# Optimization experiments

Measured on AMD Instinct MI355X. Metric: run time of the kernel, lower is better.

Reference implementation:

```python
import jax, jax.numpy as jnp
import numpy as np
import math
from jax import lax

DIM = 96
D_MODEL = 2 * DIM            # SS2D d_model
D_INNER = 2 * D_MODEL        # expand = 2
D_STATE = 16
DT_RANK = math.ceil(D_MODEL / 16)
K = 4
B_, H_, W_ = 2, 48, 48


def setup_inputs() -> dict:
    key = jax.random.key(0)
    ks = jax.random.split(key, 12)
    r = lambda k, s, sc=0.02: jax.random.normal(k, s, jnp.float32) * sc
    A = np.tile(np.arange(1, D_STATE + 1, dtype=np.float32)[None, :], (K * D_INNER, 1))
    return dict(
        x=jax.random.normal(ks[0], (B_, DIM, H_, W_), jnp.float32),
        w_init=r(ks[1], (D_MODEL, DIM)),
        b_init=r(ks[2], (D_MODEL,)),
        w_fina=r(ks[3], (DIM, D_MODEL)),
        b_fina=r(ks[4], (DIM,)),
        in_proj_w=r(ks[5], (2 * D_INNER, D_MODEL)),
        conv_w=r(ks[6], (D_INNER, 1, 3, 3), 0.1),
        conv_b=r(ks[7], (D_INNER,)),
        x_proj_w=r(ks[8], (K, DT_RANK + 2 * D_STATE, D_INNER)),
        dt_w=r(ks[9], (K, D_INNER, DT_RANK), 0.1),
        dt_b=r(ks[10], (K, D_INNER), 0.1),
        A_logs=jnp.asarray(np.log(A)),
        Ds=jnp.ones((K * D_INNER,), jnp.float32),
        ln_g=jnp.ones((D_INNER,), jnp.float32),
        ln_b=jnp.zeros((D_INNER,), jnp.float32),
        out_proj_w=r(ks[11], (D_MODEL, D_INNER)),
    )


def _gelu(x):
    return jax.nn.gelu(x, approximate=False)


def _conv1x1(x, w, b):
    # x: (b,c,h,w), w: (o,c)
    return jnp.einsum('oc,bchw->bohw', w, x) + b[None, :, None, None]


def _ss2d(x, in_proj_w, conv_w, conv_b, x_proj_w, dt_w, dt_b, A_logs, Ds, ln_g, ln_b, out_proj_w):
    # x: (b, h, w, d_model)
    b, h, w, _ = x.shape
    L = h * w
    xz = jnp.einsum('bhwc,oc->bhwo', x, in_proj_w)          # (b,h,w,2*d_inner)
    xx, z = jnp.split(xz, 2, axis=-1)
    xc = xx.transpose(0, 3, 1, 2)                            # (b, d_inner, h, w)
    xc = lax.conv_general_dilated(xc, conv_w, (1, 1), 'SAME',
                                  feature_group_count=D_INNER,
                                  dimension_numbers=('NCHW', 'OIHW', 'NCHW'))
    xc = jax.nn.silu(xc + conv_b[None, :, None, None])
    # 4 scan directions: hw, wh, reversed hw, reversed wh
    x_hw = xc.reshape(b, D_INNER, L)
    x_wh = xc.transpose(0, 1, 3, 2).reshape(b, D_INNER, L)
    xs = jnp.stack([x_hw, x_wh, x_hw[..., ::-1], x_wh[..., ::-1]], axis=1)   # (b,K,d,L)
    x_dbl = jnp.einsum('bkdl,kcd->bkcl', xs, x_proj_w)
    dts = x_dbl[:, :, :DT_RANK]                               # (b,K,r,L)
    Bs = x_dbl[:, :, DT_RANK:DT_RANK + D_STATE]               # (b,K,n,L)
    Cs = x_dbl[:, :, DT_RANK + D_STATE:]                      # (b,K,n,L)
    dts = jnp.einsum('bkrl,kdr->bkdl', dts, dt_w)
    delta = jax.nn.softplus(dts + dt_b[None, :, :, None])     # (b,K,d,L)
    A = -jnp.exp(A_logs).reshape(K, D_INNER, D_STATE)         # (K,d,n)
    Dm = Ds.reshape(K, D_INNER)
    # selective scan over L (time-major stacked inputs)
    u_t = xs.transpose(3, 0, 1, 2)      # (L,b,K,d)
    dt_t = delta.transpose(3, 0, 1, 2)  # (L,b,K,d)
    B_t = Bs.transpose(3, 0, 1, 2)      # (L,b,K,n)
    C_t = Cs.transpose(3, 0, 1, 2)      # (L,b,K,n)
    h0 = jnp.zeros((b, K, D_INNER, D_STATE), xs.dtype)

    def step(hst, inp):
        u, dt, Bv, Cv = inp
        dA = jnp.exp(dt[..., None] * A)                       # (b,K,d,n)
        hst = dA * hst + (dt * u)[..., None] * Bv[:, :, None, :]
        y = jnp.einsum('bkdn,bkn->bkd', hst, Cv)
        return hst, y

    _, ys = lax.scan(step, h0, (u_t, dt_t, B_t, C_t))         # (L,b,K,d)
    ys = ys.transpose(1, 2, 3, 0) + Dm[None, :, :, None] * xs  # (b,K,d,L)
    y1 = ys[:, 0]
    y3 = ys[:, 2][..., ::-1]
    y2 = ys[:, 1].reshape(b, D_INNER, w, h).transpose(0, 1, 3, 2).reshape(b, D_INNER, L)
    y4 = ys[:, 3][..., ::-1].reshape(b, D_INNER, w, h).transpose(0, 1, 3, 2).reshape(b, D_INNER, L)
    y = (y1 + y2 + y3 + y4).transpose(0, 2, 1).reshape(b, h, w, D_INNER)
    mu = y.mean(-1, keepdims=True)
    var = y.var(-1, keepdims=True)
    y = (y - mu) / jnp.sqrt(var + 1e-5) * ln_g + ln_b
    y = y * jax.nn.silu(z)
    return jnp.einsum('bhwd,od->bhwo', y, out_proj_w)         # (b,h,w,d_model)


def _forward(x, w_init, b_init, w_fina, b_fina, in_proj_w, conv_w, conv_b,
             x_proj_w, dt_w, dt_b, A_logs, Ds, ln_g, ln_b, out_proj_w):
    x1 = _gelu(_conv1x1(x, w_init, b_init))                   # (b,2*dim,h,w)
    x0 = x1
    xt = x1.transpose(0, 2, 3, 1)                             # b h w c
    y = _ss2d(xt, in_proj_w, conv_w, conv_b, x_proj_w, dt_w, dt_b,
              A_logs, Ds, ln_g, ln_b, out_proj_w)
    y = y.transpose(0, 3, 1, 2)
    return _gelu(_conv1x1(y + x0, w_fina, b_fina))            # (b,dim,h,w)


def reference(x, w_init, b_init, w_fina, b_fina, in_proj_w, conv_w, conv_b,
              x_proj_w, dt_w, dt_b, A_logs, Ds, ln_g, ln_b, out_proj_w):
    return _forward(x, w_init, b_init, w_fina, b_fina, in_proj_w, conv_w, conv_b,
                    x_proj_w, dt_w, dt_b, A_logs, Ds, ln_g, ln_b, out_proj_w)
```

## Files before the change

kernel.cpp:

```cpp
#include <hip/hip_runtime.h>
#include <math.h>

#define LL 2304
#define HH 48
#define WW 48
#define BB 2
#define CI 96
#define DM 192
#define DI 384
#define KK 4
#define RR 12
#define NN 16
#define KC 44
#define CH 96
#define LEN 24

typedef short bf16x8 __attribute__((ext_vector_type(8)));
typedef float f32x4 __attribute__((ext_vector_type(4)));

__device__ __forceinline__ float gelu_f(float x){
    return 0.5f*x*(1.0f+erff(x*0.70710678118654752f));
}
__device__ __forceinline__ float silu_f(float x){
    return x/(1.0f+__expf(-x));
}
__device__ __forceinline__ float softplus_f(float x){
    return fmaxf(x,0.0f) + log1pf(__expf(-fabsf(x)));
}
__device__ __forceinline__ unsigned short bf16_rne(float x){
    unsigned u = __float_as_uint(x);
    unsigned r = (u + 0x7FFFu + ((u>>16)&1u)) >> 16;
    return (unsigned short)r;
}
__device__ __forceinline__ void split_bf16(float x, unsigned short& h, unsigned short& l){
    h = bf16_rne(x);
    float fh = __uint_as_float(((unsigned)h)<<16);
    l = bf16_rne(x - fh);
}

__global__ __launch_bounds__(256) void k_convw(const float* __restrict__ ipw, const float* __restrict__ xpw,
        const float* __restrict__ opw, const float* __restrict__ wiw, const float* __restrict__ wfw,
        short* __restrict__ wh_ip, short* __restrict__ wl_ip,
        short* __restrict__ wh_xp, short* __restrict__ wl_xp,
        short* __restrict__ wh_op, short* __restrict__ wl_op,
        short* __restrict__ wh_in, short* __restrict__ wl_in,
        short* __restrict__ wh_fi, short* __restrict__ wl_fi){
    int idx = blockIdx.x*256 + threadIdx.x;
    if(idx >= 325632) return;
    unsigned short h, l;
    if(idx < 147456){
        split_bf16(ipw[idx], h, l); wh_ip[idx]=h; wl_ip[idx]=l;
    } else if(idx < 215040){
        int j = idx - 147456;
        split_bf16(xpw[j], h, l); wh_xp[j]=h; wl_xp[j]=l;
    } else if(idx < 288768){
        int j = idx - 215040;
        split_bf16(opw[j], h, l); wh_op[j]=h; wl_op[j]=l;
    } else if(idx < 307200){
        int j = idx - 288768;
        split_bf16(wiw[j], h, l); wh_in[j]=h; wl_in[j]=l;
    } else {
        int j = idx - 307200;
        split_bf16(wfw[j], h, l); wh_fi[j]=h; wl_fi[j]=l;
    }
}

template<int K>
__device__ __forceinline__ void mfma_core(const short* __restrict__ Ah, const short* __restrict__ Al,
        const short* __restrict__ Bh, const short* __restrict__ Bl, f32x4 acc[2][4]){
    int lane = threadIdx.x & 63;
    int rl = lane & 15, g = lane >> 4;
    #pragma unroll
    for(int kc=0; kc<K; kc+=32){
        bf16x8 ah[2], al[2], bh[4], bl[4];
        #pragma unroll
        for(int mi=0;mi<2;mi++){
            ah[mi] = *reinterpret_cast<const bf16x8*>(Ah + (size_t)(mi*16+rl)*K + kc + g*8);
            al[mi] = *reinterpret_cast<const bf16x8*>(Al + (size_t)(mi*16+rl)*K + kc + g*8);
        }
        #pragma unroll
        for(int ni=0;ni<4;ni++){
            bh[ni] = *reinterpret_cast<const bf16x8*>(Bh + (size_t)(ni*16+rl)*K + kc + g*8);
            bl[ni] = *reinterpret_cast<const bf16x8*>(Bl + (size_t)(ni*16+rl)*K + kc + g*8);
        }
        #pragma unroll
        for(int mi=0;mi<2;mi++){
            #pragma unroll
            for(int ni=0;ni<4;ni++){
                acc[mi][ni] = __builtin_amdgcn_mfma_f32_16x16x32_bf16(ah[mi], bh[ni], acc[mi][ni], 0,0,0);
                acc[mi][ni] = __builtin_amdgcn_mfma_f32_16x16x32_bf16(ah[mi], bl[ni], acc[mi][ni], 0,0,0);
                acc[mi][ni] = __builtin_amdgcn_mfma_f32_16x16x32_bf16(al[mi], bh[ni], acc[mi][ni], 0,0,0);
            }
        }
    }
}

__global__ __launch_bounds__(256) void k_xT(const float* __restrict__ x,
        short* __restrict__ xTh, short* __restrict__ xTl){
    __shared__ float tile[32][33];
    int b = blockIdx.z;
    int l0 = blockIdx.x*32, c0 = blockIdx.y*32;
    int tx = threadIdx.x & 31, ty = threadIdx.x >> 5;
    #pragma unroll
    for(int j=0;j<4;j++)
        tile[ty+8*j][tx] = x[((size_t)b*CI + c0+ty+8*j)*LL + l0+tx];
    __syncthreads();
    #pragma unroll
    for(int j=0;j<4;j++){
        float v = tile[tx][ty+8*j];
        size_t di = ((size_t)b*LL + l0+ty+8*j)*CI + c0+tx;
        unsigned short h,l; split_bf16(v,h,l);
        xTh[di]=(short)h; xTl[di]=(short)l;
    }
}

__global__ __launch_bounds__(256) void k_init(const short* __restrict__ wh, const short* __restrict__ wlo,
        const short* __restrict__ xTh, const short* __restrict__ xTl, const float* __restrict__ bias,
        float* __restrict__ x1, short* __restrict__ x1Th, short* __restrict__ x1Tl){
    int w = threadIdx.x >> 6, lane = threadIdx.x & 63;
    int wm = w >> 1, wn = w & 1;
    int m0 = blockIdx.y*64 + wm*32;
    int n0 = blockIdx.x*128 + wn*64;
    int b = blockIdx.z;
    f32x4 acc[2][4];
    #pragma unroll
    for(int mi=0;mi<2;mi++)
        #pragma unroll
        for(int ni=0;ni<4;ni++) acc[mi][ni] = (f32x4){0.f,0.f,0.f,0.f};
    mfma_core<CI>(wh + (size_t)m0*CI, wlo + (size_t)m0*CI,
                  xTh + ((size_t)b*LL + n0)*CI, xTl + ((size_t)b*LL + n0)*CI, acc);
    int rl = lane & 15, g = lane >> 4;
    #pragma unroll
    for(int mi=0;mi<2;mi++){
        #pragma unroll
        for(int ni=0;ni<4;ni++){
            int mb = m0 + mi*16 + g*4;
            int l = n0 + ni*16 + rl;
            unsigned hp[2], lp[2];
            #pragma unroll
            for(int i=0;i<4;i++){
                int m = mb + i;
                float v = gelu_f(acc[mi][ni][i] + bias[m]);
                x1[((size_t)b*DM + m)*LL + l] = v;
                unsigned short h, lo_;
                split_bf16(v, h, lo_);
                if(i & 1){ hp[i>>1] |= ((unsigned)h)<<16; lp[i>>1] |= ((unsigned)lo_)<<16; }
                else     { hp[i>>1] = h; lp[i>>1] = lo_; }
            }
            size_t tb = ((size_t)b*LL + l)*DM + mb;
            *reinterpret_cast<uint2*>(x1Th + tb) = make_uint2(hp[0],hp[1]);
            *reinterpret_cast<uint2*>(x1Tl + tb) = make_uint2(lp[0],lp[1]);
        }
    }
}

__global__ __launch_bounds__(256) void k_inproj(const short* __restrict__ wh, const short* __restrict__ wlo,
        const short* __restrict__ x1Th, const short* __restrict__ x1Tl,
        float* __restrict__ xx, float* __restrict__ zT){
    int w = threadIdx.x >> 6, lane = threadIdx.x & 63;
    int wm = w >> 1, wn = w & 1;
    int m0 = blockIdx.y*64 + wm*32;
    int n0 = blockIdx.x*128 + wn*64;
    int b = blockIdx.z;
    f32x4 acc[2][4];
    #pragma unroll
    for(int mi=0;mi<2;mi++)
        #pragma unroll
        for(int ni=0;ni<4;ni++) acc[mi][ni] = (f32x4){0.f,0.f,0.f,0.f};
    mfma_core<DM>(wh + (size_t)m0*DM, wlo + (size_t)m0*DM,
                  x1Th + ((size_t)b*LL + n0)*DM, x1Tl + ((size_t)b*LL + n0)*DM, acc);
    int rl = lane & 15, g = lane >> 4;
    #pragma unroll
    for(int mi=0;mi<2;mi++){
        #pragma unroll
        for(int ni=0;ni<4;ni++){
            int mb = m0 + mi*16 + g*4;
            int l = n0 + ni*16 + rl;
            if(mb < DI){
                #pragma unroll
                for(int i=0;i<4;i++)
                    xx[((size_t)b*DI + mb+i)*LL + l] = acc[mi][ni][i];
            } else {
                float4 zv = make_float4(acc[mi][ni][0], acc[mi][ni][1], acc[mi][ni][2], acc[mi][ni][3]);
                *reinterpret_cast<float4*>(zT + ((size_t)b*LL + l)*DI + (mb - DI)) = zv;
            }
        }
    }
}

__global__ __launch_bounds__(256) void k_dwconvT(const float* __restrict__ xx, const float* __restrict__ cw,
        const float* __restrict__ cb, float* __restrict__ xcT,
        short* __restrict__ xcTh, short* __restrict__ xcTl){
    __shared__ float tile[32][33];
    int b = blockIdx.z;
    int l0 = blockIdx.x*32, d0 = blockIdx.y*32;
    int tx = threadIdx.x & 31, ty = threadIdx.x >> 5;
    int l = l0 + tx;
    int h = l/WW, w = l%WW;
    #pragma unroll
    for(int j=0;j<4;j++){
        int d = d0 + ty + 8*j;
        const float* src = xx + ((size_t)b*DI + d)*LL;
        float acc = cb[d];
        #pragma unroll
        for(int dh=-1;dh<=1;dh++){
            int hh = h+dh; if(hh<0||hh>=HH) continue;
            #pragma unroll
            for(int dw=-1;dw<=1;dw++){
                int w2 = w+dw; if(w2<0||w2>=WW) continue;
                acc += cw[d*9 + (dh+1)*3 + (dw+1)] * src[hh*WW + w2];
            }
        }
        tile[ty+8*j][tx] = silu_f(acc);
    }
    __syncthreads();
    #pragma unroll
    for(int j=0;j<4;j++){
        float v = tile[tx][ty+8*j];
        size_t di = ((size_t)b*LL + l0+ty+8*j)*DI + d0+tx;
        xcT[di] = v;
        unsigned short hh,ll;
        split_bf16(v,hh,ll);
        xcTh[di] = (short)hh; xcTl[di] = (short)ll;
    }
}

__global__ __launch_bounds__(256) void k_proj(const short* __restrict__ wh, const short* __restrict__ wlo,
        const short* __restrict__ xcTh, const short* __restrict__ xcTl,
        float* __restrict__ pj){
    int w = threadIdx.x >> 6, lane = threadIdx.x & 63;
    int wm = w >> 1, wn = w & 1;
    int m0 = blockIdx.y*64 + wm*32;
    int n0 = blockIdx.x*128 + wn*64;
    int b = blockIdx.z;
    f32x4 acc[2][4];
    #pragma unroll
    for(int mi=0;mi<2;mi++)
        #pragma unroll
        for(int ni=0;ni<4;ni++) acc[mi][ni] = (f32x4){0.f,0.f,0.f,0.f};
    mfma_core<DI>(wh + (size_t)m0*DI, wlo + (size_t)m0*DI,
                  xcTh + ((size_t)b*LL + n0)*DI, xcTl + ((size_t)b*LL + n0)*DI, acc);
    int rl = lane & 15, g = lane >> 4;
    #pragma unroll
    for(int mi=0;mi<2;mi++){
        #pragma unroll
        for(int ni=0;ni<4;ni++){
            #pragma unroll
            for(int i=0;i<4;i++){
                int m = m0 + mi*16 + g*4 + i;
                if(m >= KK*KC) continue;
                int l = n0 + ni*16 + rl;
                pj[((size_t)b*(KK*KC) + m)*LL + l] = acc[mi][ni][i];
            }
        }
    }
}

__global__ __launch_bounds__(256) void k_delta(const float* __restrict__ pj, const float* __restrict__ dtw,
        const float* __restrict__ dtb, float* __restrict__ deltaT){
    __shared__ float pjs[RR*32];
    int p0 = blockIdx.x*32;
    int bk = blockIdx.z; int b = bk>>2, k = bk&3;
    int lane = threadIdx.x & 63, sub = threadIdx.x >> 6;
    int d = blockIdx.y*64 + lane;
    const float* pjb = pj + ((size_t)b*(KK*KC) + k*KC)*LL;
    for(int idx=threadIdx.x; idx<RR*32; idx+=256){
        int r = idx>>5, pp = idx&31;
        pjs[idx] = pjb[(size_t)r*LL + p0+pp];
    }
    __syncthreads();
    float wr[RR];
    #pragma unroll
    for(int r=0;r<RR;r++) wr[r] = dtw[((size_t)k*DI + d)*RR + r];
    float dtbv = dtb[k*DI + d];
    #pragma unroll
    for(int i=0;i<8;i++){
        int pp = sub*8+i;
        float acc = dtbv;
        #pragma unroll
        for(int r=0;r<RR;r++) acc += wr[r]*pjs[r*32+pp];
        deltaT[((size_t)bk*LL + p0+pp)*DI + d] = softplus_f(acc);
    }
}

__device__ __forceinline__ int perm_pos(int k, int l){
    int lk = (k>=2) ? (LL-1-l) : l;
    return (k&1) ? ((lk%WW)*WW + lk/WW) : lk;
}
__device__ __forceinline__ void dA_powers(float dt, float dA[NN]){
    float e1 = __expf(-dt);
    float e2=e1*e1, e3=e2*e1, e4=e2*e2;
    float e5=e4*e1, e6=e4*e2, e7=e4*e3, e8=e4*e4;
    dA[0]=e1; dA[1]=e2; dA[2]=e3; dA[3]=e4; dA[4]=e5; dA[5]=e6; dA[6]=e7; dA[7]=e8;
    dA[8]=e8*e1; dA[9]=e8*e2; dA[10]=e8*e3; dA[11]=e8*e4;
    dA[12]=e8*e5; dA[13]=e8*e6; dA[14]=e8*e7; dA[15]=e8*e8;
}

__global__ __launch_bounds__(384) void k_scan1(const float* __restrict__ xcT, const float* __restrict__ pj,
        const float* __restrict__ deltaT,
        float* __restrict__ gbuf, float* __restrict__ Sbuf){
    __shared__ float bs[LEN*16];
    int chunk = blockIdx.x;
    int bk = blockIdx.y; int b = bk>>2, k = bk&3;
    int lane = threadIdx.x & 63, wv = threadIdx.x >> 6;
    int d = wv*64 + lane;
    const float* pjb = pj + ((size_t)b*(KK*KC) + k*KC)*LL;
    for(int idx=threadIdx.x; idx<LEN*16; idx+=384){
        int s = idx>>4, n = idx&15;
        int p = perm_pos(k, chunk*LEN+s);
        bs[idx] = pjb[(size_t)(RR+n)*LL + p];
    }
    __syncthreads();
    float h[NN];
    #pragma unroll
    for(int n=0;n<NN;n++) h[n]=0.f;
    float S = 0.f;
    const float* dptr = deltaT + (size_t)bk*LL*DI + d;
    const float* uptr = xcT + (size_t)b*LL*DI + d;
    int pn = perm_pos(k, chunk*LEN);
    float dtn = dptr[(size_t)pn*DI];
    float un  = uptr[(size_t)pn*DI];
    for(int s=0;s<LEN;s++){
        float dt = dtn, u = un;
        if(s+1 < LEN){
            int p2 = perm_pos(k, chunk*LEN+s+1);
            dtn = dptr[(size_t)p2*DI];
            un  = uptr[(size_t)p2*DI];
        }
        S += dt;
        float du = dt*u;
        float dA[NN];
        dA_powers(dt, dA);
        #pragma unroll
        for(int nq=0;nq<4;nq++){
            float4 Bq = *reinterpret_cast<const float4*>(bs + s*16 + nq*4);
            h[nq*4+0] = fmaf(h[nq*4+0], dA[nq*4+0], du*Bq.x);
            h[nq*4+1] = fmaf(h[nq*4+1], dA[nq*4+1], du*Bq.y);
            h[nq*4+2] = fmaf(h[nq*4+2], dA[nq*4+2], du*Bq.z);
            h[nq*4+3] = fmaf(h[nq*4+3], dA[nq*4+3], du*Bq.w);
        }
    }
    int base = (bk*CH + chunk)*NN;
    #pragma unroll
    for(int n=0;n<NN;n++) gbuf[(size_t)(base+n)*DI + d] = h[n];
    Sbuf[(size_t)(bk*CH + chunk)*DI + d] = S;
}

__global__ __launch_bounds__(128) void k_scan2(const float* __restrict__ alogs, const float* __restrict__ Sbuf,
        float* __restrict__ gbuf){
    int id = blockIdx.x*128 + threadIdx.x;
    int d = id % DI;
    int n = (id/DI) % NN;
    int bk = id/(DI*NN);
    int k = bk & 3;
    float a = -__expf(alogs[((size_t)k*DI + d)*NN + n]);
    float h = 0.f;
    for(int j=0;j<CH;j++){
        float S = Sbuf[(size_t)(bk*CH + j)*DI + d];
        size_t gi = (size_t)((bk*CH + j)*NN + n)*DI + d;
        float g = gbuf[gi];
        gbuf[gi] = h;
        h = __expf(a*S)*h + g;
    }
}

__global__ __launch_bounds__(384) void k_scan3(const float* __restrict__ xcT, const float* __restrict__ pj,
        const float* __restrict__ deltaT,
        const float* __restrict__ gbuf, float* __restrict__ yout){
    __shared__ float bs[LEN*32];
    int chunk = blockIdx.x;
    int bk = blockIdx.y; int b = bk>>2, k = bk&3;
    int lane = threadIdx.x & 63, wv = threadIdx.x >> 6;
    int d = wv*64 + lane;
    const float* pjb = pj + ((size_t)b*(KK*KC) + k*KC)*LL;
    for(int idx=threadIdx.x; idx<LEN*32; idx+=384){
        int s = idx>>5, c = idx&31;
        int p = perm_pos(k, chunk*LEN+s);
        bs[idx] = pjb[(size_t)(RR+c)*LL + p];
    }
    __syncthreads();
    float h[NN];
    int base = (bk*CH + chunk)*NN;
    #pragma unroll
    for(int n=0;n<NN;n++) h[n] = gbuf[(size_t)(base+n)*DI + d];
    const float* dptr = deltaT + (size_t)bk*LL*DI + d;
    const float* uptr = xcT + (size_t)b*LL*DI + d;
    float* yptr = yout + (size_t)bk*LL*DI + d;
    int pn = perm_pos(k, chunk*LEN);
    float dtn = dptr[(size_t)pn*DI];
    float un  = uptr[(size_t)pn*DI];
    for(int s=0;s<LEN;s++){
        float dt = dtn, u = un;
        int p = pn;
        if(s+1 < LEN){
            pn = perm_pos(k, chunk*LEN+s+1);
            dtn = dptr[(size_t)pn*DI];
            un  = uptr[(size_t)pn*DI];
        }
        float du = dt*u;
        float dA[NN];
        dA_powers(dt, dA);
        float y = 0.f;
        #pragma unroll
        for(int nq=0;nq<4;nq++){
            float4 Bq = *reinterpret_cast<const float4*>(bs + s*32 + nq*4);
            float4 Cq = *reinterpret_cast<const float4*>(bs + s*32 + 16 + nq*4);
            h[nq*4+0] = fmaf(h[nq*4+0], dA[nq*4+0], du*Bq.x);  y = fmaf(h[nq*4+0], Cq.x, y);
            h[nq*4+1] = fmaf(h[nq*4+1], dA[nq*4+1], du*Bq.y);  y = fmaf(h[nq*4+1], Cq.y, y);
            h[nq*4+2] = fmaf(h[nq*4+2], dA[nq*4+2], du*Bq.z);  y = fmaf(h[nq*4+2], Cq.z, y);
            h[nq*4+3] = fmaf(h[nq*4+3], dA[nq*4+3], du*Bq.w);  y = fmaf(h[nq*4+3], Cq.w, y);
        }
        yptr[(size_t)p*DI] = y;
    }
}

__global__ __launch_bounds__(256) void k_merge(const float* __restrict__ yout, const float* __restrict__ xcT,
        const float* __restrict__ zT, const float* __restrict__ Ds,
        const float* __restrict__ lng, const float* __restrict__ lnb,
        short* __restrict__ ygh, short* __restrict__ ygl){
    __shared__ float tile[32*385];
    int p0 = blockIdx.x*32; int b = blockIdx.y;
    for(int idx=threadIdx.x; idx<32*DI; idx+=256){
        int pp = idx/DI, d = idx%DI; int p = p0+pp;
        float dsum = Ds[d] + Ds[DI+d] + Ds[2*DI+d] + Ds[3*DI+d];
        float v = dsum * xcT[((size_t)b*LL + p)*DI + d];
        #pragma unroll
        for(int kk=0;kk<4;kk++) v += yout[((size_t)(b*4+kk)*LL + p)*DI + d];
        tile[pp*385 + d] = v;
    }
    __syncthreads();
    int lane = threadIdx.x & 63, wv = threadIdx.x >> 6;
    for(int i=0;i<8;i++){
        int pp = wv*8 + i; int p = p0+pp;
        float s1=0.f, s2=0.f;
        float vals[6];
        #pragma unroll
        for(int j=0;j<6;j++){ float v = tile[pp*385 + lane + 64*j]; vals[j]=v; s1+=v; s2+=v*v; }
        #pragma unroll
        for(int m=1;m<64;m<<=1){ s1 += __shfl_xor(s1,m); s2 += __shfl_xor(s2,m); }
        float mu = s1*(1.0f/DI);
        float var = s2*(1.0f/DI) - mu*mu;
        float rstd = rsqrtf(var + 1e-5f);
        #pragma unroll
        for(int j=0;j<6;j++){
            int c = lane + 64*j;
            float zv = zT[((size_t)b*LL + p)*DI + c];
            float y = (vals[j]-mu)*rstd*lng[c] + lnb[c];
            float gv = y * silu_f(zv);
            unsigned short h,l;
            split_bf16(gv,h,l);
            size_t oi = ((size_t)b*LL + p)*DI + c;
            ygh[oi] = (short)h; ygl[oi] = (short)l;
        }
    }
}

__global__ __launch_bounds__(256) void k_outproj(const short* __restrict__ wh, const short* __restrict__ wlo,
        const short* __restrict__ ygh, const short* __restrict__ ygl,
        const float* __restrict__ x1, short* __restrict__ yoTh, short* __restrict__ yoTl){
    int w = threadIdx.x >> 6, lane = threadIdx.x & 63;
    int wm = w >> 1, wn = w & 1;
    int m0 = blockIdx.y*64 + wm*32;
    int n0 = blockIdx.x*128 + wn*64;
    int b = blockIdx.z;
    f32x4 acc[2][4];
    #pragma unroll
    for(int mi=0;mi<2;mi++)
        #pragma unroll
        for(int ni=0;ni<4;ni++) acc[mi][ni] = (f32x4){0.f,0.f,0.f,0.f};
    mfma_core<DI>(wh + (size_t)m0*DI, wlo + (size_t)m0*DI,
                  ygh + ((size_t)b*LL + n0)*DI, ygl + ((size_t)b*LL + n0)*DI, acc);
    int rl = lane & 15, g = lane >> 4;
    #pragma unroll
    for(int mi=0;mi<2;mi++){
        #pragma unroll
        for(int ni=0;ni<4;ni++){
            int mb = m0 + mi*16 + g*4;
            int l = n0 + ni*16 + rl;
            unsigned hp[2], lp[2];
            #pragma unroll
            for(int i=0;i<4;i++){
                int m = mb + i;
                float v = acc[mi][ni][i] + x1[((size_t)b*DM + m)*LL + l];
                unsigned short h, lo_;
                split_bf16(v, h, lo_);
                if(i & 1){ hp[i>>1] |= ((unsigned)h)<<16; lp[i>>1] |= ((unsigned)lo_)<<16; }
                else     { hp[i>>1] = h; lp[i>>1] = lo_; }
            }
            size_t tb = ((size_t)b*LL + l)*DM + mb;
            *reinterpret_cast<uint2*>(yoTh + tb) = make_uint2(hp[0],hp[1]);
            *reinterpret_cast<uint2*>(yoTl + tb) = make_uint2(lp[0],lp[1]);
        }
    }
}

__global__ __launch_bounds__(256) void k_final(const short* __restrict__ wh, const short* __restrict__ wlo,
        const short* __restrict__ yoTh, const short* __restrict__ yoTl, const float* __restrict__ bias,
        float* __restrict__ out){
    int w = threadIdx.x >> 6, lane = threadIdx.x & 63;
    int wm = w >> 1, wn = w & 1;
    int m0 = blockIdx.y*64 + wm*32;
    int n0 = blockIdx.x*128 + wn*64;
    int b = blockIdx.z;
    f32x4 acc[2][4];
    #pragma unroll
    for(int mi=0;mi<2;mi++)
        #pragma unroll
        for(int ni=0;ni<4;ni++) acc[mi][ni] = (f32x4){0.f,0.f,0.f,0.f};
    mfma_core<DM>(wh + (size_t)m0*DM, wlo + (size_t)m0*DM,
                  yoTh + ((size_t)b*LL + n0)*DM, yoTl + ((size_t)b*LL + n0)*DM, acc);
    int rl = lane & 15, g = lane >> 4;
    #pragma unroll
    for(int mi=0;mi<2;mi++){
        #pragma unroll
        for(int ni=0;ni<4;ni++){
            #pragma unroll
            for(int i=0;i<4;i++){
                int m = m0 + mi*16 + g*4 + i;
                if(m >= CI) continue;
                int l = n0 + ni*16 + rl;
                out[((size_t)b*CI + m)*LL + l] = gelu_f(acc[mi][ni][i] + bias[m]);
            }
        }
    }
}

extern "C" void kernel_launch(void* const* d_in, const int* in_sizes, int n_in,
                              void* d_out, int out_size, void* d_ws, size_t ws_size,
                              hipStream_t stream) {
    const float* x        = (const float*)d_in[0];
    const float* w_init   = (const float*)d_in[1];
    const float* b_init   = (const float*)d_in[2];
    const float* w_fina   = (const float*)d_in[3];
    const float* b_fina   = (const float*)d_in[4];
    const float* in_proj_w= (const float*)d_in[5];
    const float* conv_w   = (const float*)d_in[6];
    const float* conv_b   = (const float*)d_in[7];
    const float* x_proj_w = (const float*)d_in[8];
    const float* dt_w     = (const float*)d_in[9];
    const float* dt_b     = (const float*)d_in[10];
    const float* A_logs   = (const float*)d_in[11];
    const float* Ds       = (const float*)d_in[12];
    const float* ln_g     = (const float*)d_in[13];
    const float* ln_b     = (const float*)d_in[14];
    const float* out_proj_w=(const float*)d_in[15];

    float* ws   = (float*)d_ws;
    float* x1   = ws;
    float* xx   = x1 + 884736;
    float* xcT  = xx + 1769472;
    float* zT   = xcT+ 1769472;
    float* pj   = zT + 1769472;
    float* yout = pj + 811008;
    float* gbuf = yout + 7077888;
    float* Sbuf = gbuf + 4718592;
    float* deltaT = Sbuf + 294912;
    short* sb   = (short*)(deltaT + 7077888);
    short* wh_ip = sb;            short* wl_ip = wh_ip + 147456;
    short* wh_xp = wl_ip+147456;  short* wl_xp = wh_xp + 73728;
    short* wh_op = wl_xp+73728;   short* wl_op = wh_op + 73728;
    short* wh_in = wl_op+73728;   short* wl_in = wh_in + 18432;
    short* wh_fi = wl_in+18432;   short* wl_fi = wh_fi + 18432;
    short* xTh   = wl_fi+18432;   short* xTl   = xTh + 442368;
    short* x1Th  = xTl+442368;    short* x1Tl  = x1Th + 884736;
    short* xcTh  = x1Tl+884736;   short* xcTl  = xcTh + 1769472;
    short* ygh   = xcTl+1769472;  short* ygl   = ygh + 1769472;
    short* yoTh  = ygl+1769472;   short* yoTl  = yoTh + 884736;

    dim3 blk(256);
    k_convw  <<<dim3(1272), blk, 0, stream>>>(in_proj_w, x_proj_w, out_proj_w, w_init, w_fina,
                                              wh_ip, wl_ip, wh_xp, wl_xp, wh_op, wl_op,
                                              wh_in, wl_in, wh_fi, wl_fi);
    k_xT     <<<dim3(72,3,BB), blk, 0, stream>>>(x, xTh, xTl);
    k_init   <<<dim3(18,3,BB), blk, 0, stream>>>(wh_in, wl_in, xTh, xTl, b_init, x1, x1Th, x1Tl);
    k_inproj <<<dim3(18,12,BB), blk, 0, stream>>>(wh_ip, wl_ip, x1Th, x1Tl, xx, zT);
    k_dwconvT<<<dim3(72,12,BB), blk, 0, stream>>>(xx, conv_w, conv_b, xcT, xcTh, xcTl);
    k_proj   <<<dim3(18,3,BB), blk, 0, stream>>>(wh_xp, wl_xp, xcTh, xcTl, pj);
    k_delta  <<<dim3(72,6,BB*KK), blk, 0, stream>>>(pj, dt_w, dt_b, deltaT);
    k_scan1  <<<dim3(CH,BB*KK), dim3(384), 0, stream>>>(xcT, pj, deltaT, gbuf, Sbuf);
    k_scan2  <<<dim3(384), dim3(128), 0, stream>>>(A_logs, Sbuf, gbuf);
    k_scan3  <<<dim3(CH,BB*KK), dim3(384), 0, stream>>>(xcT, pj, deltaT, gbuf, yout);
    k_merge  <<<dim3(72,BB), blk, 0, stream>>>(yout, xcT, zT, Ds, ln_g, ln_b, ygh, ygl);
    k_outproj<<<dim3(18,3,BB), blk, 0, stream>>>(wh_op, wl_op, ygh, ygl, x1, yoTh, yoTl);
    k_final  <<<dim3(18,2,BB), blk, 0, stream>>>(wh_fi, wl_fi, yoTh, yoTl, b_fina, (float*)d_out);
}
```

Measured before the change: 297.4 us.

## Merge weight split with input transpose; prefetch exp and split scan reduction

Folds the input transpose/bf16-split kernel into the weight-conversion kernel, removing one launch. In both scan kernels, the exp(-dt) for the next step is computed alongside the prefetched loads, taking it off the dependent chain. In the output scan, the single serial y accumulation chain becomes four independent partial sums. Results can differ slightly from the different summation order.

```diff
diff --git a/kernel.cpp b/kernel.cpp
--- a/kernel.cpp
+++ b/kernel.cpp
@@ -38,30 +38,51 @@
     l = bf16_rne(x - fh);
 }
 
-__global__ __launch_bounds__(256) void k_convw(const float* __restrict__ ipw, const float* __restrict__ xpw,
+__global__ __launch_bounds__(256) void k_pre(const float* __restrict__ ipw, const float* __restrict__ xpw,
         const float* __restrict__ opw, const float* __restrict__ wiw, const float* __restrict__ wfw,
+        const float* __restrict__ x,
         short* __restrict__ wh_ip, short* __restrict__ wl_ip,
         short* __restrict__ wh_xp, short* __restrict__ wl_xp,
         short* __restrict__ wh_op, short* __restrict__ wl_op,
         short* __restrict__ wh_in, short* __restrict__ wl_in,
-        short* __restrict__ wh_fi, short* __restrict__ wl_fi){
-    int idx = blockIdx.x*256 + threadIdx.x;
-    if(idx >= 325632) return;
-    unsigned short h, l;
-    if(idx < 147456){
-        split_bf16(ipw[idx], h, l); wh_ip[idx]=h; wl_ip[idx]=l;
-    } else if(idx < 215040){
-        int j = idx - 147456;
-        split_bf16(xpw[j], h, l); wh_xp[j]=h; wl_xp[j]=l;
-    } else if(idx < 288768){
-        int j = idx - 215040;
-        split_bf16(opw[j], h, l); wh_op[j]=h; wl_op[j]=l;
-    } else if(idx < 307200){
-        int j = idx - 288768;
-        split_bf16(wiw[j], h, l); wh_in[j]=h; wl_in[j]=l;
+        short* __restrict__ wh_fi, short* __restrict__ wl_fi,
+        short* __restrict__ xTh, short* __restrict__ xTl){
+    __shared__ float tile[32][33];
+    if(blockIdx.x < 1272){
+        int idx = blockIdx.x*256 + threadIdx.x;
+        if(idx >= 325632) return;
+        unsigned short h, l;
+        if(idx < 147456){
+            split_bf16(ipw[idx], h, l); wh_ip[idx]=h; wl_ip[idx]=l;
+        } else if(idx < 215040){
+            int j = idx - 147456;
+            split_bf16(xpw[j], h, l); wh_xp[j]=h; wl_xp[j]=l;
+        } else if(idx < 288768){
+            int j = idx - 215040;
+            split_bf16(opw[j], h, l); wh_op[j]=h; wl_op[j]=l;
+        } else if(idx < 307200){
+            int j = idx - 288768;
+            split_bf16(wiw[j], h, l); wh_in[j]=h; wl_in[j]=l;
+        } else {
+            int j = idx - 307200;
+            split_bf16(wfw[j], h, l); wh_fi[j]=h; wl_fi[j]=l;
+        }
     } else {
-        int j = idx - 307200;
-        split_bf16(wfw[j], h, l); wh_fi[j]=h; wl_fi[j]=l;
+        int id = blockIdx.x - 1272;
+        int bx = id % 72, by = (id/72) % 3, b = id/216;
+        int l0 = bx*32, c0 = by*32;
+        int tx = threadIdx.x & 31, ty = threadIdx.x >> 5;
+        #pragma unroll
+        for(int j=0;j<4;j++)
+            tile[ty+8*j][tx] = x[((size_t)b*CI + c0+ty+8*j)*LL + l0+tx];
+        __syncthreads();
+        #pragma unroll
+        for(int j=0;j<4;j++){
+            float v = tile[tx][ty+8*j];
+            size_t di = ((size_t)b*LL + l0+ty+8*j)*CI + c0+tx;
+            unsigned short h,l; split_bf16(v,h,l);
+            xTh[di]=(short)h; xTl[di]=(short)l;
+        }
     }
 }
 
@@ -92,25 +113,6 @@
                 acc[mi][ni] = __builtin_amdgcn_mfma_f32_16x16x32_bf16(al[mi], bh[ni], acc[mi][ni], 0,0,0);
             }
         }
-    }
-}
-
-__global__ __launch_bounds__(256) void k_xT(const float* __restrict__ x,
-        short* __restrict__ xTh, short* __restrict__ xTl){
-    __shared__ float tile[32][33];
-    int b = blockIdx.z;
-    int l0 = blockIdx.x*32, c0 = blockIdx.y*32;
-    int tx = threadIdx.x & 31, ty = threadIdx.x >> 5;
-    #pragma unroll
-    for(int j=0;j<4;j++)
-        tile[ty+8*j][tx] = x[((size_t)b*CI + c0+ty+8*j)*LL + l0+tx];
-    __syncthreads();
-    #pragma unroll
-    for(int j=0;j<4;j++){
-        float v = tile[tx][ty+8*j];
-        size_t di = ((size_t)b*LL + l0+ty+8*j)*CI + c0+tx;
-        unsigned short h,l; split_bf16(v,h,l);
-        xTh[di]=(short)h; xTl[di]=(short)l;
     }
 }
 
@@ -287,8 +289,7 @@
     int lk = (k>=2) ? (LL-1-l) : l;
     return (k&1) ? ((lk%WW)*WW + lk/WW) : lk;
 }
-__device__ __forceinline__ void dA_powers(float dt, float dA[NN]){
-    float e1 = __expf(-dt);
+__device__ __forceinline__ void dA_from_e1(float e1, float dA[NN]){
     float e2=e1*e1, e3=e2*e1, e4=e2*e2;
     float e5=e4*e1, e6=e4*e2, e7=e4*e3, e8=e4*e4;
     dA[0]=e1; dA[1]=e2; dA[2]=e3; dA[3]=e4; dA[4]=e5; dA[5]=e6; dA[6]=e7; dA[7]=e8;
@@ -320,17 +321,19 @@
     int pn = perm_pos(k, chunk*LEN);
     float dtn = dptr[(size_t)pn*DI];
     float un  = uptr[(size_t)pn*DI];
+    float e1n = __expf(-dtn);
     for(int s=0;s<LEN;s++){
-        float dt = dtn, u = un;
+        float dt = dtn, u = un, e1 = e1n;
         if(s+1 < LEN){
             int p2 = perm_pos(k, chunk*LEN+s+1);
             dtn = dptr[(size_t)p2*DI];
             un  = uptr[(size_t)p2*DI];
+            e1n = __expf(-dtn);
         }
         S += dt;
         float du = dt*u;
         float dA[NN];
-        dA_powers(dt, dA);
+        dA_from_e1(e1, dA);
         #pragma unroll
         for(int nq=0;nq<4;nq++){
             float4 Bq = *reinterpret_cast<const float4*>(bs + s*16 + nq*4);
@@ -389,28 +392,53 @@
     int pn = perm_pos(k, chunk*LEN);
     float dtn = dptr[(size_t)pn*DI];
     float un  = uptr[(size_t)pn*DI];
+    float e1n = __expf(-dtn);
     for(int s=0;s<LEN;s++){
-        float dt = dtn, u = un;
+        float dt = dtn, u = un, e1 = e1n;
         int p = pn;
         if(s+1 < LEN){
             pn = perm_pos(k, chunk*LEN+s+1);
             dtn = dptr[(size_t)pn*DI];
             un  = uptr[(size_t)pn*DI];
+            e1n = __expf(-dtn);
         }
         float du = dt*u;
         float dA[NN];
-        dA_powers(dt, dA);
-        float y = 0.f;
-        #pragma unroll
-        for(int nq=0;nq<4;nq++){
-            float4 Bq = *reinterpret_cast<const float4*>(bs + s*32 + nq*4);
-            float4 Cq = *reinterpret_cast<const float4*>(bs + s*32 + 16 + nq*4);
-            h[nq*4+0] = fmaf(h[nq*4+0], dA[nq*4+0], du*Bq.x);  y = fmaf(h[nq*4+0], Cq.x, y);
-            h[nq*4+1] = fmaf(h[nq*4+1], dA[nq*4+1], du*Bq.y);  y = fmaf(h[nq*4+1], Cq.y, y);
-            h[nq*4+2] = fmaf(h[nq*4+2], dA[nq*4+2], du*Bq.z);  y = fmaf(h[nq*4+2], Cq.z, y);
-            h[nq*4+3] = fmaf(h[nq*4+3], dA[nq*4+3], du*Bq.w);  y = fmaf(h[nq*4+3], Cq.w, y);
-        }
-        yptr[(size_t)p*DI] = y;
+        dA_from_e1(e1, dA);
+        float y0=0.f, y1=0.f, y2=0.f, y3=0.f;
+        {
+            float4 Bq = *reinterpret_cast<const float4*>(bs + s*32 + 0);
+            float4 Cq = *reinterpret_cast<const float4*>(bs + s*32 + 16);
+            h[0] = fmaf(h[0], dA[0], du*Bq.x);  y0 = fmaf(h[0], Cq.x, y0);
+            h[1] = fmaf(h[1], dA[1], du*Bq.y);  y1 = fmaf(h[1], Cq.y, y1);
+            h[2] = fmaf(h[2], dA[2], du*Bq.z);  y2 = fmaf(h[2], Cq.z, y2);
+            h[3] = fmaf(h[3], dA[3], du*Bq.w);  y3 = fmaf(h[3], Cq.w, y3);
+        }
+        {
+            float4 Bq = *reinterpret_cast<const float4*>(bs + s*32 + 4);
+            float4 Cq = *reinterpret_cast<const float4*>(bs + s*32 + 20);
+            h[4] = fmaf(h[4], dA[4], du*Bq.x);  y0 = fmaf(h[4], Cq.x, y0);
+            h[5] = fmaf(h[5], dA[5], du*Bq.y);  y1 = fmaf(h[5], Cq.y, y1);
+            h[6] = fmaf(h[6], dA[6], du*Bq.z);  y2 = fmaf(h[6], Cq.z, y2);
+            h[7] = fmaf(h[7], dA[7], du*Bq.w);  y3 = fmaf(h[7], Cq.w, y3);
+        }
+        {
+            float4 Bq = *reinterpret_cast<const float4*>(bs + s*32 + 8);
+            float4 Cq = *reinterpret_cast<const float4*>(bs + s*32 + 24);
+            h[8]  = fmaf(h[8],  dA[8],  du*Bq.x);  y0 = fmaf(h[8],  Cq.x, y0);
+            h[9]  = fmaf(h[9],  dA[9],  du*Bq.y);  y1 = fmaf(h[9],  Cq.y, y1);
+            h[10] = fmaf(h[10], dA[10], du*Bq.z);  y2 = fmaf(h[10], Cq.z, y2);
+            h[11] = fmaf(h[11], dA[11], du*Bq.w);  y3 = fmaf(h[11], Cq.w, y3);
+        }
+        {
+            float4 Bq = *reinterpret_cast<const float4*>(bs + s*32 + 12);
+            float4 Cq = *reinterpret_cast<const float4*>(bs + s*32 + 28);
+            h[12] = fmaf(h[12], dA[12], du*Bq.x);  y0 = fmaf(h[12], Cq.x, y0);
+            h[13] = fmaf(h[13], dA[13], du*Bq.y);  y1 = fmaf(h[13], Cq.y, y1);
+            h[14] = fmaf(h[14], dA[14], du*Bq.z);  y2 = fmaf(h[14], Cq.z, y2);
+            h[15] = fmaf(h[15], dA[15], du*Bq.w);  y3 = fmaf(h[15], Cq.w, y3);
+        }
+        yptr[(size_t)p*DI] = (y0+y1)+(y2+y3);
     }
 }
 
@@ -568,10 +596,9 @@
     short* yoTh  = ygl+1769472;   short* yoTl  = yoTh + 884736;
 
     dim3 blk(256);
-    k_convw  <<<dim3(1272), blk, 0, stream>>>(in_proj_w, x_proj_w, out_proj_w, w_init, w_fina,
+    k_pre    <<<dim3(1704), blk, 0, stream>>>(in_proj_w, x_proj_w, out_proj_w, w_init, w_fina, x,
                                               wh_ip, wl_ip, wh_xp, wl_xp, wh_op, wl_op,
-                                              wh_in, wl_in, wh_fi, wl_fi);
-    k_xT     <<<dim3(72,3,BB), blk, 0, stream>>>(x, xTh, xTl);
+                                              wh_in, wl_in, wh_fi, wl_fi, xTh, xTl);
     k_init   <<<dim3(18,3,BB), blk, 0, stream>>>(wh_in, wl_in, xTh, xTl, b_init, x1, x1Th, x1Tl);
     k_inproj <<<dim3(18,12,BB), blk, 0, stream>>>(wh_ip, wl_ip, x1Th, x1Tl, xx, zT);
     k_dwconvT<<<dim3(72,12,BB), blk, 0, stream>>>(xx, conv_w, conv_b, xcT, xcTh, xcTl);
```

Result: no change. 298.1 us, median of 2 (+0.3%).
